# Kernel tuning notes

Hardware: AMD Instinct MI355X
Metric: run time of the kernel (lower is better)

## Reference

```python
import jax, jax.numpy as jnp
import numpy as np
import math

D = 768
H = 8
DK = D // H
FF = 1024
EPS = 1e-5


def _layer_norm(x, g, b):
    m = jnp.mean(x, axis=-1, keepdims=True)
    v = jnp.mean((x - m) ** 2, axis=-1, keepdims=True)
    return (x - m) * jax.lax.rsqrt(v + EPS) * g + b


def _mha(x, attention_mask, Wq, bq, Wv, bv, g, b):
    # x: (B,S,D); attention_mask: (B,S,1) bool (True = masked/padding query row)
    B, S, _ = x.shape
    q = (x @ Wq + bq).reshape(B, S, H, DK).transpose(0, 2, 1, 3)  # (B,H,S,dk)
    # NOTE: original code uses the V projection for BOTH k and v (k = self.V(x))
    kv = (x @ Wv + bv).reshape(B, S, H, DK).transpose(0, 2, 1, 3)
    k = kv
    v = kv
    w = jnp.einsum('bhqd,bhkd->bhqk', q, k) / math.sqrt(DK)  # (B,H,S,S)
    pad = attention_mask[:, None, :, :]                      # (B,1,S,1) -> bcast (B,1,S,S)
    causal = jnp.triu(jnp.ones((S, S), dtype=bool), k=1)     # look-ahead mask
    mask = pad | causal
    w = jnp.where(mask, jnp.float32(-1e9), w)
    # NOTE: original uses nn.Softmax(dim=2) -> softmax over the QUERY axis
    score = jax.nn.softmax(w, axis=2)
    o = jnp.einsum('bhqk,bhkd->bhqd', score, v)              # (B,H,S,dk)
    o = o.transpose(0, 2, 1, 3).reshape(B, S, D)
    return _layer_norm(o + x, g, b)


def _ffn(x, W1, b1, W2, b2, g, b):
    h = jax.nn.relu(x @ W1 + b1)
    return _layer_norm(h @ W2 + b2 + x, g, b)


def setup_inputs() -> dict:
    key = jax.random.key(0)
    ks = jax.random.split(key, 16)
    B, S = 8, 1024
    sc = 0.02
    inp = {
        'x': jax.random.normal(ks[0], (B, S, D), dtype=jnp.float32),
        'attention_mask': jax.random.randint(ks[1], (B, S, 1), 0, 2).astype(bool),
    }
    for i, pre in enumerate(['a1', 'a2']):
        inp[pre + '_Wq'] = jax.random.normal(ks[2 + 4 * i], (D, D), dtype=jnp.float32) * sc
        inp[pre + '_bq'] = jnp.zeros((D,), dtype=jnp.float32)
        inp[pre + '_Wv'] = jax.random.normal(ks[3 + 4 * i], (D, D), dtype=jnp.float32) * sc
        inp[pre + '_bv'] = jnp.zeros((D,), dtype=jnp.float32)
        inp[pre + '_g'] = jnp.ones((D,), dtype=jnp.float32)
        inp[pre + '_b'] = jnp.zeros((D,), dtype=jnp.float32)
    inp['f_W1'] = jax.random.normal(ks[10], (D, FF), dtype=jnp.float32) * sc
    inp['f_b1'] = jnp.zeros((FF,), dtype=jnp.float32)
    inp['f_W2'] = jax.random.normal(ks[11], (FF, D), dtype=jnp.float32) * sc
    inp['f_b2'] = jnp.zeros((D,), dtype=jnp.float32)
    inp['f_g'] = jnp.ones((D,), dtype=jnp.float32)
    inp['f_b'] = jnp.zeros((D,), dtype=jnp.float32)
    return inp


def reference(x, attention_mask,
              a1_Wq, a1_bq, a1_Wv, a1_bv, a1_g, a1_b,
              a2_Wq, a2_bq, a2_Wv, a2_bv, a2_g, a2_b,
              f_W1, f_b1, f_W2, f_b2, f_g, f_b):
    x = _mha(x, attention_mask, a1_Wq, a1_bq, a1_Wv, a1_bv, a1_g, a1_b)
    x = _mha(x, attention_mask, a2_Wq, a2_bq, a2_Wv, a2_bv, a2_g, a2_b)
    x = _ffn(x, f_W1, f_b1, f_W2, f_b2, f_g, f_b)
    return x
```

## Files before the change

kernel.cpp:

```cpp
#include <hip/hip_runtime.h>
#include <cstddef>

#define BB 8
#define SS 1024
#define DD 768
#define HH 8
#define DKK 96
#define FFF 1024
#define MM (BB*SS)
#define QVW 1536
#define SM_SCALE 0.10206207261596577f
#define NT2 8

typedef unsigned short ushort_t;
typedef short short8 __attribute__((ext_vector_type(8)));
typedef float f32x4 __attribute__((ext_vector_type(4)));
typedef float f32x16 __attribute__((ext_vector_type(16)));
typedef ushort_t us4 __attribute__((ext_vector_type(4)));
typedef unsigned uint2v __attribute__((ext_vector_type(2)));

__device__ __forceinline__ ushort_t f2b(float f) {
    union { float f; unsigned u; } x; x.f = f;
    unsigned r = x.u + 0x7fffu + ((x.u >> 16) & 1u);
    return (ushort_t)(r >> 16);
}
__device__ __forceinline__ float b2f(ushort_t u) {
    union { unsigned u; float f; } x; x.u = ((unsigned)u) << 16;
    return x.f;
}
__device__ __forceinline__ void gload16(const ushort_t* g, void* lds_base) {
    __builtin_amdgcn_global_load_lds(
        (const __attribute__((address_space(1))) unsigned int*)g,
        (__attribute__((address_space(3))) unsigned int*)lds_base, 16, 0, 0);
}
__device__ __forceinline__ void plswap(unsigned& a, unsigned& b) {
#if __has_builtin(__builtin_amdgcn_permlane32_swap)
    uint2v r = __builtin_amdgcn_permlane32_swap(a, b, false, false);
    a = r[0]; b = r[1];
#else
    asm("v_permlane32_swap_b32 %0, %1" : "+v"(a), "+v"(b));
#endif
}

__device__ __forceinline__ void castWT_body(
    const float* __restrict__ W, ushort_t* __restrict__ Wt,
    int K, int N, int bx, int by)
{
    __shared__ float T[32][33];
    const int tx = threadIdx.x & 31, ty = threadIdx.x >> 5;
    const int n0 = bx * 32, k0 = by * 32;
    #pragma unroll
    for (int r = 0; r < 4; ++r)
        T[ty + 8*r][tx] = W[(size_t)(k0 + ty + 8*r) * N + n0 + tx];
    __syncthreads();
    #pragma unroll
    for (int r = 0; r < 4; ++r)
        Wt[(size_t)(n0 + ty + 8*r) * K + k0 + tx] = f2b(T[tx][ty + 8*r]);
}

__global__ __launch_bounds__(256) void prep_all(
    const float* __restrict__ Wqa, const float* __restrict__ Wva,
    const float* __restrict__ Wqb, const float* __restrict__ Wvb,
    ushort_t* __restrict__ Tqa, ushort_t* __restrict__ Tva,
    ushort_t* __restrict__ Tqb, ushort_t* __restrict__ Tvb,
    const float* __restrict__ W1, ushort_t* __restrict__ T1,
    const float* __restrict__ W2, ushort_t* __restrict__ T2,
    const float* __restrict__ x, ushort_t* __restrict__ xb)
{
    const int id = blockIdx.x;
    if (id < 2304) {
        const int z = id / 576, r = id % 576;
        const float* W = (z == 0) ? Wqa : (z == 1) ? Wva : (z == 2) ? Wqb : Wvb;
        ushort_t* Wt   = (z == 0) ? Tqa : (z == 1) ? Tva : (z == 2) ? Tqb : Tvb;
        castWT_body(W, Wt, DD, DD, r % 24, r / 24);
    } else if (id < 3072) {
        const int r = id - 2304;
        castWT_body(W1, T1, DD, FFF, r % 32, r / 32);
    } else if (id < 3840) {
        const int r = id - 3072;
        castWT_body(W2, T2, FFF, DD, r % 24, r / 24);
    } else {
        const int i = (id - 3840) * 256 + threadIdx.x;
        const float4 v = ((const float4*)x)[i];
        us4 o; o.x = f2b(v.x); o.y = f2b(v.y); o.z = f2b(v.z); o.w = f2b(v.w);
        ((us4*)xb)[i] = o;
    }
}

template<int RELU>
__global__ __launch_bounds__(256) void gemm_bt(
    const ushort_t* __restrict__ A, const ushort_t* __restrict__ Bt,
    const float* __restrict__ bias, const float* __restrict__ bias2, int bN,
    ushort_t* __restrict__ C, int K, int N)
{
    __shared__ ushort_t S[4*128*64];
    const int tid  = threadIdx.x;
    const int lane = tid & 63, wave = tid >> 6;
    const int wm = wave >> 1, wn = wave & 1;
    const int n = lane & 15, quad = lane >> 4;
    const int sx = n & 7;
    const int nbx = N >> 7;
    const int cpx = gridDim.x >> 3;
    const int sw  = (blockIdx.x & 7) * cpx + (blockIdx.x >> 3);
    const int bm = (sw / nbx) * 128, bn = (sw % nbx) * 128;

    f32x4 acc[4][4];
    #pragma unroll
    for (int i = 0; i < 4; ++i)
        #pragma unroll
        for (int j = 0; j < 4; ++j) acc[i][j] = (f32x4){0.f, 0.f, 0.f, 0.f};

    auto stage = [&](int k0, int buf) {
        char* abase = (char*)S + buf * 16384;
        char* bbase = (char*)S + 32768 + buf * 16384;
        #pragma unroll
        for (int it = 0; it < 4; ++it) {
            const int u   = (it*4 + wave)*64 + lane;
            const int row = u >> 3;
            const int c   = (u & 7) ^ (row & 7);
            gload16(A  + (size_t)(bm + row) * K + k0 + c*8, abase + (it*4 + wave)*1024);
            gload16(Bt + (size_t)(bn + row) * K + k0 + c*8, bbase + (it*4 + wave)*1024);
        }
    };

    stage(0, 0);
    __syncthreads();
    int cur = 0;
    for (int k0 = 0; k0 < K; k0 += 64) {
        if (k0 + 64 < K) stage(k0 + 64, cur ^ 1);
        const ushort_t* As = S + cur * 8192;
        const ushort_t* Bs = S + 16384 + cur * 8192;
        #pragma unroll
        for (int ks = 0; ks < 2; ++ks) {
            short8 af[4], bf[4];
            #pragma unroll
            for (int i = 0; i < 4; ++i)
                af[i] = *(short8*)&As[((wm*64 + i*16 + n)*8 + ((ks*4 + quad) ^ sx))*8];
            #pragma unroll
            for (int j = 0; j < 4; ++j)
                bf[j] = *(short8*)&Bs[((wn*64 + j*16 + n)*8 + ((ks*4 + quad) ^ sx))*8];
            __builtin_amdgcn_s_setprio(1);
            #pragma unroll
            for (int i = 0; i < 4; ++i)
                #pragma unroll
                for (int j = 0; j < 4; ++j)
                    acc[i][j] = __builtin_amdgcn_mfma_f32_16x16x32_bf16(af[i], bf[j], acc[i][j], 0, 0, 0);
            __builtin_amdgcn_s_setprio(0);
        }
        __syncthreads();
        cur ^= 1;
    }
    #pragma unroll
    for (int j = 0; j < 4; ++j) {
        const int col = wn*64 + j*16 + n;
        const int gcol = bn + col;
        const float bsv = (gcol < bN) ? bias[gcol] : bias2[gcol - bN];
        #pragma unroll
        for (int i = 0; i < 4; ++i) {
            const int lrow = wm*64 + i*16 + quad*4;
            #pragma unroll
            for (int r = 0; r < 4; ++r) {
                float v = acc[i][j][r] + bsv;
                if (RELU) v = fmaxf(v, 0.f);
                S[(lrow + r)*136 + col] = f2b(v);
            }
        }
    }
    __syncthreads();
    #pragma unroll
    for (int it = 0; it < 8; ++it) {
        const int u = it*256 + tid;
        const int grow = u >> 4, gc = u & 15;
        *(short8*)(C + (size_t)(bm + grow)*N + bn + gc*8) = *(short8*)&S[grow*136 + gc*8];
    }
}

__global__ __launch_bounds__(512) void attn_sums(
    const ushort_t* __restrict__ QV, const int* __restrict__ amask,
    float* __restrict__ lpart)
{
    __shared__ ushort_t Qs[128*128];
    __shared__ ushort_t Ks[2][64*128];
    __shared__ float colsum[2][8][64];
    const int tid = threadIdx.x, lane = tid & 63, wave = tid >> 6;
    const int n = lane & 15, quad = lane >> 4, sx = n & 7;
    const int hwid = blockIdx.x;
    const int v = (hwid & 7) * 32 + (hwid >> 3);
    const int px = v & 3, h = (v >> 2) & 7, b = v >> 5;
    const ushort_t* Qh = QV + (size_t)b*SS*QVW + h*DKK;
    const ushort_t* Kh = QV + (size_t)b*SS*QVW + DD + h*DKK;
    float* lpq = lpart + (size_t)(b*HH + h)*NT2*SS;

    #pragma unroll
    for (int half = 0; half < 2; ++half) {
        const int qt2 = half ? (7 - px) : px;
        const int q0 = qt2 * 128;
        const int ktmax = 2*qt2 + 1;
        #pragma unroll
        for (int it = 0; it < 4; ++it) {
            const int u = (it*8 + wave)*64 + lane;
            const int row = u >> 4, c = (u & 15) ^ (row & 7);
            if (c < 12)
                gload16(Qh + (size_t)(q0 + row)*QVW + c*8, (char*)Qs + (it*8 + wave)*1024);
        }
        const int4 mv = *(const int4*)&amask[b*SS + q0 + wave*16 + quad*4];
        const int mr[4] = {mv.x, mv.y, mv.z, mv.w};
        #pragma unroll
        for (int it = 0; it < 2; ++it) {
            const int u = (it*8 + wave)*64 + lane;
            const int row = u >> 4, c = (u & 15) ^ (row & 7);
            if (c < 12)
                gload16(Kh + (size_t)row*QVW + c*8, (char*)Ks[0] + (it*8 + wave)*1024);
        }
        __syncthreads();
        short8 aq[3];
        #pragma unroll
        for (int ks = 0; ks < 3; ++ks)
            aq[ks] = *(short8*)&Qs[((wave*16 + n)*16 + ((ks*4 + quad) ^ sx))*8];

        int cur = 0;
        for (int kt = 0; kt <= ktmax; ++kt) {
            const int k0 = kt * 64;
            if (kt < ktmax) {
                #pragma unroll
                for (int it = 0; it < 2; ++it) {
                    const int u = (it*8 + wave)*64 + lane;
                    const int row = u >> 4, c = (u & 15) ^ (row & 7);
                    if (c < 12)
                        gload16(Kh + (size_t)(k0 + 64 + row)*QVW + c*8,
                                (char*)Ks[cur^1] + (it*8 + wave)*1024);
                }
            }
            if (kt > 0 && tid < 64) {
                const float s = colsum[cur^1][0][tid] + colsum[cur^1][1][tid]
                              + colsum[cur^1][2][tid] + colsum[cur^1][3][tid]
                              + colsum[cur^1][4][tid] + colsum[cur^1][5][tid]
                              + colsum[cur^1][6][tid] + colsum[cur^1][7][tid];
                lpq[(size_t)qt2*SS + (k0 - 64) + tid] = s;
            }
            #pragma unroll
            for (int ns = 0; ns < 4; ++ns) {
                f32x4 sa = (f32x4){0.f, 0.f, 0.f, 0.f};
                __builtin_amdgcn_s_setprio(1);
                #pragma unroll
                for (int ks = 0; ks < 3; ++ks) {
                    const short8 bk = *(short8*)&Ks[cur][((ns*16 + n)*16 + ((ks*4 + quad) ^ sx))*8];
                    sa = __builtin_amdgcn_mfma_f32_16x16x32_bf16(aq[ks], bk, sa, 0, 0, 0);
                }
                __builtin_amdgcn_s_setprio(0);
                const int kl = ns*16 + n;
                const int keyg = k0 + kl;
                float s = 0.f;
                #pragma unroll
                for (int r = 0; r < 4; ++r) {
                    const int qg = q0 + wave*16 + quad*4 + r;
                    const bool dead = (mr[r] != 0) || (keyg > qg);
                    s += dead ? 0.f : __expf(sa[r] * SM_SCALE);
                }
                s += __shfl_xor(s, 16);
                s += __shfl_xor(s, 32);
                if (quad == 0) colsum[cur][wave][kl] = s;
            }
            __syncthreads();
            cur ^= 1;
        }
        if (tid < 64) {
            const int pb = ktmax & 1;
            const float s = colsum[pb][0][tid] + colsum[pb][1][tid]
                          + colsum[pb][2][tid] + colsum[pb][3][tid]
                          + colsum[pb][4][tid] + colsum[pb][5][tid]
                          + colsum[pb][6][tid] + colsum[pb][7][tid];
            lpq[(size_t)qt2*SS + ktmax*64 + tid] = s;
        }
    }
}

__global__ __launch_bounds__(256) void transpose_scale(
    const ushort_t* __restrict__ QV, const float* __restrict__ lpart,
    ushort_t* __restrict__ Vt)
{
    __shared__ ushort_t T[64][104];
    __shared__ float rlv[64];
    const int tid = threadIdx.x;
    const int k0 = blockIdx.x * 64, h = blockIdx.y, b = blockIdx.z;
    const ushort_t* src = QV + (size_t)b*SS*QVW + DD + h*DKK;
    for (int s = tid; s < 768; s += 256) {
        const int r = s / 12, c = s % 12;
        *(short8*)&T[r][c*8] = *(const short8*)(src + (size_t)(k0 + r)*QVW + c*8);
    }
    if (tid < 64) {
        const float* lp = lpart + (size_t)(b*HH + h)*NT2*SS;
        float l = 0.f;
        for (int qt2 = k0 >> 7; qt2 < NT2; ++qt2) l += lp[(size_t)qt2*SS + k0 + tid];
        rlv[tid] = (l > 0.f) ? (1.f / l) : 0.f;
    }
    __syncthreads();
    ushort_t* dst = Vt + ((size_t)b*HH + h)*DKK*SS;
    for (int s = tid; s < 768; s += 256) {
        const int dk = s >> 3, c = s & 7;
        short8 v;
        #pragma unroll
        for (int i = 0; i < 8; ++i)
            v[i] = (short)f2b(b2f(T[c*8 + i][dk]) * rlv[c*8 + i]);
        *(short8*)(dst + (size_t)dk*SS + k0 + c*8) = v;
    }
}

__global__ __launch_bounds__(512, 1) void attn_pv_re(
    const ushort_t* __restrict__ QV, const int* __restrict__ amask,
    const ushort_t* __restrict__ Vt, ushort_t* __restrict__ O)
{
    __shared__ ushort_t Ks[2][2][64*128];
    __shared__ ushort_t Vs[2][2][96*64];
    const int tid = threadIdx.x, lane = tid & 63, wave = tid >> 6;
    const int grp = wave >> 2, w4 = wave & 3;
    const int ln31 = lane & 31, hi = lane >> 5;
    const int hwid = blockIdx.x;
    const int v = (hwid & 7) * 32 + (hwid >> 3);
    const int px = v & 3, h = (v >> 2) & 7, b = v >> 5;
    const ushort_t* Qh = QV + (size_t)b*SS*QVW + h*DKK;
    const ushort_t* Kh = QV + (size_t)b*SS*QVW + DD + h*DKK;
    const ushort_t* Vth = Vt + ((size_t)b*HH + h)*DKK*SS;

    const int qt2 = grp ? (7 - px) : px;
    const int q0 = qt2 * 128;
    const int ktmax = 2*qt2 + 1;
    const int ktend = 2*(7 - px) + 1;
    const int qrow = q0 + w4*32 + ln31;
    short8 bq[6];
    #pragma unroll
    for (int t = 0; t < 6; ++t)
        bq[t] = *(const short8*)(Qh + (size_t)qrow*QVW + t*16 + hi*8);
    const bool padq = amask[b*SS + qrow] != 0;

    #pragma unroll
    for (int it = 0; it < 4; ++it) {
        const int u = (it*4 + w4)*64 + lane;
        const int row = u >> 4, c = (u & 15) ^ (row & 7);
        if (c < 12)
            gload16(Kh + (size_t)row*QVW + c*8, (char*)Ks[grp][0] + (it*4 + w4)*1024);
    }
    #pragma unroll
    for (int it = 0; it < 3; ++it) {
        const int u = (it*4 + w4)*64 + lane;
        const int row = u >> 3, c = (u & 7) ^ (row & 7);
        gload16(Vth + (size_t)row*SS + c*8, (char*)Vs[grp][0] + (it*4 + w4)*1024);
    }
    __syncthreads();

    f32x16 acc[3];
    #pragma unroll
    for (int db = 0; db < 3; ++db)
        #pragma unroll
        for (int i = 0; i < 16; ++i) acc[db][i] = 0.f;

    int cur = 0;
    for (int kt = 0; kt <= ktend; ++kt) {
        const int k0 = kt * 64;
        if (kt < ktmax) {
            #pragma unroll
            for (int it = 0; it < 4; ++it) {
                const int u = (it*4 + w4)*64 + lane;
                const int row = u >> 4, c = (u & 15) ^ (row & 7);
                if (c < 12)
                    gload16(Kh + (size_t)(k0 + 64 + row)*QVW + c*8,
                            (char*)Ks[grp][cur^1] + (it*4 + w4)*1024);
            }
            #pragma unroll
            for (int it = 0; it < 3; ++it) {
                const int u = (it*4 + w4)*64 + lane;
                const int row = u >> 3, c = (u & 7) ^ (row & 7);
                gload16(Vth + (size_t)row*SS + k0 + 64 + c*8,
                        (char*)Vs[grp][cur^1] + (it*4 + w4)*1024);
            }
        }
        if (kt <= ktmax) {
            #pragma unroll
            for (int kb = 0; kb < 2; ++kb) {
                f32x16 sk;
                #pragma unroll
                for (int i = 0; i < 16; ++i) sk[i] = 0.f;
                const int krow = kb*32 + ln31;
                __builtin_amdgcn_s_setprio(1);
                #pragma unroll
                for (int t = 0; t < 6; ++t) {
                    const short8 ak = *(short8*)&Ks[grp][cur][krow*128 + (((t*2 + hi) ^ (krow & 7))*8)];
                    sk = __builtin_amdgcn_mfma_f32_32x32x16_bf16(ak, bq[t], sk, 0, 0, 0);
                }
                __builtin_amdgcn_s_setprio(0);
                const int kbase = k0 + kb*32 + 4*hi;
                float p[16];
                #pragma unroll
                for (int r = 0; r < 16; ++r) {
                    const int kg = kbase + (r & 3) + 8*(r >> 2);
                    const bool dead = padq || (kg > qrow);
                    p[r] = dead ? 0.f : __expf(sk[r] * SM_SCALE);
                }
                unsigned w[8];
                #pragma unroll
                for (int i = 0; i < 8; ++i)
                    asm("v_cvt_pk_bf16_f32 %0, %1, %2" : "=v"(w[i]) : "v"(p[2*i]), "v"(p[2*i+1]));
                plswap(w[0], w[2]);
                plswap(w[1], w[3]);
                plswap(w[4], w[6]);
                plswap(w[5], w[7]);
                __builtin_amdgcn_s_setprio(1);
                #pragma unroll
                for (int s = 0; s < 2; ++s) {
                    short8 ae;
                    unsigned* aeu = (unsigned*)&ae;
                    aeu[0] = w[s*4 + 0]; aeu[1] = w[s*4 + 1];
                    aeu[2] = w[s*4 + 2]; aeu[3] = w[s*4 + 3];
                    #pragma unroll
                    for (int db = 0; db < 3; ++db) {
                        const int drow = db*32 + ln31;
                        const short8 bv = *(short8*)&Vs[grp][cur][drow*64 + (((kb*4 + s*2 + hi) ^ (drow & 7))*8)];
                        acc[db] = __builtin_amdgcn_mfma_f32_32x32x16_bf16(ae, bv, acc[db], 0, 0, 0);
                    }
                }
                __builtin_amdgcn_s_setprio(0);
            }
        }
        __syncthreads();
        cur ^= 1;
    }
    #pragma unroll
    for (int db = 0; db < 3; ++db) {
        #pragma unroll
        for (int r = 0; r < 16; ++r) {
            const int q = q0 + w4*32 + (r & 3) + 8*(r >> 2) + 4*hi;
            O[((size_t)b*SS + q)*DD + h*DKK + db*32 + ln31] = f2b(acc[db][r]);
        }
    }
}

__device__ __forceinline__ float block_sum256(float s, float* tmp4)
{
    #pragma unroll
    for (int off = 32; off > 0; off >>= 1) s += __shfl_down(s, off);
    __syncthreads();
    if ((threadIdx.x & 63) == 0) tmp4[threadIdx.x >> 6] = s;
    __syncthreads();
    return tmp4[0] + tmp4[1] + tmp4[2] + tmp4[3];
}

template<int XBF, int RBF, int OUTF32>
__global__ __launch_bounds__(256) void resid_ln(
    const void* __restrict__ X, const void* __restrict__ R,
    const float* __restrict__ g, const float* __restrict__ beta,
    ushort_t* __restrict__ OutB, float* __restrict__ OutF)
{
    __shared__ float tmp4[4];
    const int row = blockIdx.x;
    const int tid = threadIdx.x;
    float v[3], s = 0.f;
    #pragma unroll
    for (int i = 0; i < 3; ++i) {
        const size_t idx = (size_t)row * DD + tid + 256*i;
        const float xv = XBF ? b2f(((const ushort_t*)X)[idx]) : ((const float*)X)[idx];
        const float rv = RBF ? b2f(((const ushort_t*)R)[idx]) : ((const float*)R)[idx];
        v[i] = xv + rv;
        s += v[i];
    }
    const float mu = block_sum256(s, tmp4) * (1.f / DD);
    float qv = 0.f;
    #pragma unroll
    for (int i = 0; i < 3; ++i) { const float d = v[i] - mu; qv += d * d; }
    const float inv = rsqrtf(block_sum256(qv, tmp4) * (1.f / DD) + 1e-5f);
    #pragma unroll
    for (int i = 0; i < 3; ++i) {
        const int c = tid + 256*i;
        const float o = (v[i] - mu) * inv * g[c] + beta[c];
        if (OUTF32) OutF[(size_t)row * DD + c] = o;
        else        OutB[(size_t)row * DD + c] = f2b(o);
    }
}

extern "C" void kernel_launch(void* const* d_in, const int* in_sizes, int n_in,
                              void* d_out, int out_size, void* d_ws, size_t ws_size,
                              hipStream_t stream)
{
    (void)in_sizes; (void)n_in; (void)out_size; (void)ws_size;
    const float* x0    = (const float*)d_in[0];
    const int*   amask = (const int*)d_in[1];
    const float* a1_Wq = (const float*)d_in[2];
    const float* a1_bq = (const float*)d_in[3];
    const float* a1_Wv = (const float*)d_in[4];
    const float* a1_bv = (const float*)d_in[5];
    const float* a1_g  = (const float*)d_in[6];
    const float* a1_b  = (const float*)d_in[7];
    const float* a2_Wq = (const float*)d_in[8];
    const float* a2_bq = (const float*)d_in[9];
    const float* a2_Wv = (const float*)d_in[10];
    const float* a2_bv = (const float*)d_in[11];
    const float* a2_g  = (const float*)d_in[12];
    const float* a2_b  = (const float*)d_in[13];
    const float* f_W1  = (const float*)d_in[14];
    const float* f_b1  = (const float*)d_in[15];
    const float* f_W2  = (const float*)d_in[16];
    const float* f_b2  = (const float*)d_in[17];
    const float* f_g   = (const float*)d_in[18];
    const float* f_b   = (const float*)d_in[19];

    char* ws = (char*)d_ws;
    size_t off = 0;
    auto alloc = [&](size_t bytes) { void* p = ws + off; off += (bytes + 255) & ~(size_t)255; return p; };
    ushort_t* WqvT1 = (ushort_t*)alloc((size_t)QVW*DD*2);
    ushort_t* WqvT2 = (ushort_t*)alloc((size_t)QVW*DD*2);
    ushort_t* W1T   = (ushort_t*)alloc((size_t)DD*FFF*2);
    ushort_t* W2T   = (ushort_t*)alloc((size_t)DD*FFF*2);
    ushort_t* xb0   = (ushort_t*)alloc((size_t)MM*DD*2);
    ushort_t* xb1   = (ushort_t*)alloc((size_t)MM*DD*2);
    ushort_t* xb2   = (ushort_t*)alloc((size_t)MM*DD*2);
    ushort_t* Ob    = (ushort_t*)alloc((size_t)MM*DD*2);
    ushort_t* QVb   = (ushort_t*)alloc((size_t)MM*QVW*2);
    ushort_t* hb    = QVb;
    ushort_t* Vtb   = (ushort_t*)alloc((size_t)MM*DD*2);
    float* lpart = (float*)alloc((size_t)BB*HH*NT2*SS*4);
    float* out = (float*)d_out;

    const dim3 blk(256);
    const dim3 blk512(512);
    const dim3 gat(256);
    const dim3 gtr(SS/64, HH, BB);

    prep_all<<<dim3(9984), blk, 0, stream>>>(
        a1_Wq, a1_Wv, a2_Wq, a2_Wv,
        WqvT1, WqvT1 + (size_t)DD*DD, WqvT2, WqvT2 + (size_t)DD*DD,
        f_W1, W1T, f_W2, W2T, x0, xb0);

    gemm_bt<0><<<dim3((QVW/128)*(MM/128)), blk, 0, stream>>>(xb0, WqvT1, a1_bq, a1_bv, DD, QVb, DD, QVW);
    attn_sums<<<gat, blk512, 0, stream>>>(QVb, amask, lpart);
    transpose_scale<<<gtr, blk, 0, stream>>>(QVb, lpart, Vtb);
    attn_pv_re<<<gat, blk512, 0, stream>>>(QVb, amask, Vtb, Ob);
    resid_ln<1,0,0><<<dim3(MM), blk, 0, stream>>>(Ob, x0, a1_g, a1_b, xb1, nullptr);

    gemm_bt<0><<<dim3((QVW/128)*(MM/128)), blk, 0, stream>>>(xb1, WqvT2, a2_bq, a2_bv, DD, QVb, DD, QVW);
    attn_sums<<<gat, blk512, 0, stream>>>(QVb, amask, lpart);
    transpose_scale<<<gtr, blk, 0, stream>>>(QVb, lpart, Vtb);
    attn_pv_re<<<gat, blk512, 0, stream>>>(QVb, amask, Vtb, Ob);
    resid_ln<1,1,0><<<dim3(MM), blk, 0, stream>>>(Ob, xb1, a2_g, a2_b, xb2, nullptr);

    gemm_bt<1><<<dim3((FFF/128)*(MM/128)), blk, 0, stream>>>(xb2, W1T, f_b1, f_b1, FFF, hb, DD, FFF);
    gemm_bt<0><<<dim3((DD/128)*(MM/128)), blk, 0, stream>>>(hb, W2T, f_b2, f_b2, DD, Ob, FFF, DD);
    resid_ln<1,1,1><<<dim3(MM), blk, 0, stream>>>(Ob, xb2, f_g, f_b, nullptr, out);
}
```

Baseline: 372.4 us.

## Restructure attn_sums into two concurrent wave groups with 32x32 MFMA tiles

The column-sum kernel previously processed its two query tiles one after another, using eight waves with 16x16 MFMAs and Q staged through shared memory. Now two groups of four waves each take one query tile concurrently, with their own double-buffered K tiles. Q fragments load straight into registers and scores come from 32x32x16 MFMAs. Both attention kernels also split the dot-product accumulation across two independent accumulators to break the MFMA dependency chain. The trade-off is an unbalanced group workload (the short tile idles at barriers), more registers with launch_bounds(512,1), and extra adds before the exp.

After: 377.9 us. No clear change (+1.5%).

```diff
diff --git a/kernel.cpp b/kernel.cpp
--- a/kernel.cpp
+++ b/kernel.cpp
@@ -175,15 +175,15 @@
     }
 }
 
-__global__ __launch_bounds__(512) void attn_sums(
+__global__ __launch_bounds__(512, 1) void attn_sums(
     const ushort_t* __restrict__ QV, const int* __restrict__ amask,
     float* __restrict__ lpart)
 {
-    __shared__ ushort_t Qs[128*128];
-    __shared__ ushort_t Ks[2][64*128];
-    __shared__ float colsum[2][8][64];
+    __shared__ ushort_t Ks[2][2][64*128];
+    __shared__ float colsum[2][2][4][64];
     const int tid = threadIdx.x, lane = tid & 63, wave = tid >> 6;
-    const int n = lane & 15, quad = lane >> 4, sx = n & 7;
+    const int grp = wave >> 2, w4 = wave & 3;
+    const int ln31 = lane & 31, hi = lane >> 5;
     const int hwid = blockIdx.x;
     const int v = (hwid & 7) * 32 + (hwid >> 3);
     const int px = v & 3, h = (v >> 2) & 7, b = v >> 5;
@@ -191,87 +191,81 @@
     const ushort_t* Kh = QV + (size_t)b*SS*QVW + DD + h*DKK;
     float* lpq = lpart + (size_t)(b*HH + h)*NT2*SS;
 
-    #pragma unroll
-    for (int half = 0; half < 2; ++half) {
-        const int qt2 = half ? (7 - px) : px;
-        const int q0 = qt2 * 128;
-        const int ktmax = 2*qt2 + 1;
-        #pragma unroll
-        for (int it = 0; it < 4; ++it) {
-            const int u = (it*8 + wave)*64 + lane;
-            const int row = u >> 4, c = (u & 15) ^ (row & 7);
-            if (c < 12)
-                gload16(Qh + (size_t)(q0 + row)*QVW + c*8, (char*)Qs + (it*8 + wave)*1024);
-        }
-        const int4 mv = *(const int4*)&amask[b*SS + q0 + wave*16 + quad*4];
-        const int mr[4] = {mv.x, mv.y, mv.z, mv.w};
-        #pragma unroll
-        for (int it = 0; it < 2; ++it) {
-            const int u = (it*8 + wave)*64 + lane;
-            const int row = u >> 4, c = (u & 15) ^ (row & 7);
-            if (c < 12)
-                gload16(Kh + (size_t)row*QVW + c*8, (char*)Ks[0] + (it*8 + wave)*1024);
-        }
-        __syncthreads();
-        short8 aq[3];
-        #pragma unroll
-        for (int ks = 0; ks < 3; ++ks)
-            aq[ks] = *(short8*)&Qs[((wave*16 + n)*16 + ((ks*4 + quad) ^ sx))*8];
-
-        int cur = 0;
-        for (int kt = 0; kt <= ktmax; ++kt) {
-            const int k0 = kt * 64;
-            if (kt < ktmax) {
-                #pragma unroll
-                for (int it = 0; it < 2; ++it) {
-                    const int u = (it*8 + wave)*64 + lane;
-                    const int row = u >> 4, c = (u & 15) ^ (row & 7);
-                    if (c < 12)
-                        gload16(Kh + (size_t)(k0 + 64 + row)*QVW + c*8,
-                                (char*)Ks[cur^1] + (it*8 + wave)*1024);
-                }
+    const int qt2 = grp ? (7 - px) : px;
+    const int q0 = qt2 * 128;
+    const int ktmax = 2*qt2 + 1;
+    const int ktend = 2*(7 - px) + 1;
+    short8 aq[6];
+    #pragma unroll
+    for (int t = 0; t < 6; ++t)
+        aq[t] = *(const short8*)(Qh + (size_t)(q0 + w4*32 + ln31)*QVW + t*16 + hi*8);
+    int4 mr[4];
+    #pragma unroll
+    for (int m = 0; m < 4; ++m)
+        mr[m] = *(const int4*)&amask[b*SS + q0 + w4*32 + 8*m + 4*hi];
+
+    #pragma unroll
+    for (int it = 0; it < 4; ++it) {
+        const int u = (it*4 + w4)*64 + lane;
+        const int row = u >> 4, c = (u & 15) ^ (row & 7);
+        if (c < 12)
+            gload16(Kh + (size_t)row*QVW + c*8, (char*)Ks[grp][0] + (it*4 + w4)*1024);
+    }
+    __syncthreads();
+
+    int cur = 0;
+    for (int kt = 0; kt <= ktend; ++kt) {
+        const int k0 = kt * 64;
+        if (kt < ktmax) {
+            #pragma unroll
+            for (int it = 0; it < 4; ++it) {
+                const int u = (it*4 + w4)*64 + lane;
+                const int row = u >> 4, c = (u & 15) ^ (row & 7);
+                if (c < 12)
+                    gload16(Kh + (size_t)(k0 + 64 + row)*QVW + c*8,
+                            (char*)Ks[grp][cur^1] + (it*4 + w4)*1024);
             }
-            if (kt > 0 && tid < 64) {
-                const float s = colsum[cur^1][0][tid] + colsum[cur^1][1][tid]
-                              + colsum[cur^1][2][tid] + colsum[cur^1][3][tid]
-                              + colsum[cur^1][4][tid] + colsum[cur^1][5][tid]
-                              + colsum[cur^1][6][tid] + colsum[cur^1][7][tid];
-                lpq[(size_t)qt2*SS + (k0 - 64) + tid] = s;
-            }
-            #pragma unroll
-            for (int ns = 0; ns < 4; ++ns) {
-                f32x4 sa = (f32x4){0.f, 0.f, 0.f, 0.f};
+        }
+        if (kt > 0 && kt <= ktmax + 1 && w4 == 0) {
+            const float s = colsum[grp][cur^1][0][lane] + colsum[grp][cur^1][1][lane]
+                          + colsum[grp][cur^1][2][lane] + colsum[grp][cur^1][3][lane];
+            lpq[(size_t)qt2*SS + (k0 - 64) + lane] = s;
+        }
+        if (kt <= ktmax) {
+            #pragma unroll
+            for (int kb = 0; kb < 2; ++kb) {
+                f32x16 s0, s1;
+                #pragma unroll
+                for (int i = 0; i < 16; ++i) { s0[i] = 0.f; s1[i] = 0.f; }
+                const int krow = kb*32 + ln31;
                 __builtin_amdgcn_s_setprio(1);
                 #pragma unroll
-                for (int ks = 0; ks < 3; ++ks) {
-                    const short8 bk = *(short8*)&Ks[cur][((ns*16 + n)*16 + ((ks*4 + quad) ^ sx))*8];
-                    sa = __builtin_amdgcn_mfma_f32_16x16x32_bf16(aq[ks], bk, sa, 0, 0, 0);
+                for (int t = 0; t < 6; ++t) {
+                    const short8 bk = *(short8*)&Ks[grp][cur][krow*128 + (((t*2 + hi) ^ (krow & 7))*8)];
+                    if (t & 1) s1 = __builtin_amdgcn_mfma_f32_32x32x16_bf16(aq[t], bk, s1, 0, 0, 0);
+                    else       s0 = __builtin_amdgcn_mfma_f32_32x32x16_bf16(aq[t], bk, s0, 0, 0, 0);
                 }
                 __builtin_amdgcn_s_setprio(0);
-                const int kl = ns*16 + n;
-                const int keyg = k0 + kl;
+                const int keyg = k0 + kb*32 + ln31;
                 float s = 0.f;
                 #pragma unroll
-                for (int r = 0; r < 4; ++r) {
-                    const int qg = q0 + wave*16 + quad*4 + r;
-                    const bool dead = (mr[r] != 0) || (keyg > qg);
-                    s += dead ? 0.f : __expf(sa[r] * SM_SCALE);
+                for (int r = 0; r < 16; ++r) {
+                    const int qg = q0 + w4*32 + (r & 3) + 8*(r >> 2) + 4*hi;
+                    const bool dead = ((&mr[r >> 2].x)[r & 3] != 0) || (keyg > qg);
+                    s += dead ? 0.f : __expf((s0[r] + s1[r]) * SM_SCALE);
                 }
-                s += __shfl_xor(s, 16);
                 s += __shfl_xor(s, 32);
-                if (quad == 0) colsum[cur][wave][kl] = s;
+                if (hi == 0) colsum[grp][cur][w4][kb*32 + ln31] = s;
             }
-            __syncthreads();
-            cur ^= 1;
-        }
-        if (tid < 64) {
-            const int pb = ktmax & 1;
-            const float s = colsum[pb][0][tid] + colsum[pb][1][tid]
-                          + colsum[pb][2][tid] + colsum[pb][3][tid]
-                          + colsum[pb][4][tid] + colsum[pb][5][tid]
-                          + colsum[pb][6][tid] + colsum[pb][7][tid];
-            lpq[(size_t)qt2*SS + ktmax*64 + tid] = s;
-        }
+        }
+        __syncthreads();
+        cur ^= 1;
+    }
+    if (grp == 1 && w4 == 0) {
+        const int pb = ktend & 1;
+        const float s = colsum[1][pb][0][lane] + colsum[1][pb][1][lane]
+                      + colsum[1][pb][2][lane] + colsum[1][pb][3][lane];
+        lpq[(size_t)qt2*SS + ktend*64 + lane] = s;
     }
 }
 
@@ -377,15 +371,16 @@
         if (kt <= ktmax) {
             #pragma unroll
             for (int kb = 0; kb < 2; ++kb) {
-                f32x16 sk;
-                #pragma unroll
-                for (int i = 0; i < 16; ++i) sk[i] = 0.f;
+                f32x16 s0, s1;
+                #pragma unroll
+                for (int i = 0; i < 16; ++i) { s0[i] = 0.f; s1[i] = 0.f; }
                 const int krow = kb*32 + ln31;
                 __builtin_amdgcn_s_setprio(1);
                 #pragma unroll
                 for (int t = 0; t < 6; ++t) {
                     const short8 ak = *(short8*)&Ks[grp][cur][krow*128 + (((t*2 + hi) ^ (krow & 7))*8)];
-                    sk = __builtin_amdgcn_mfma_f32_32x32x16_bf16(ak, bq[t], sk, 0, 0, 0);
+                    if (t & 1) s1 = __builtin_amdgcn_mfma_f32_32x32x16_bf16(ak, bq[t], s1, 0, 0, 0);
+                    else       s0 = __builtin_amdgcn_mfma_f32_32x32x16_bf16(ak, bq[t], s0, 0, 0, 0);
                 }
                 __builtin_amdgcn_s_setprio(0);
                 const int kbase = k0 + kb*32 + 4*hi;
@@ -394,7 +389,7 @@
                 for (int r = 0; r < 16; ++r) {
                     const int kg = kbase + (r & 3) + 8*(r >> 2);
                     const bool dead = padq || (kg > qrow);
-                    p[r] = dead ? 0.f : __expf(sk[r] * SM_SCALE);
+                    p[r] = dead ? 0.f : __expf((s0[r] + s1[r]) * SM_SCALE);
                 }
                 unsigned w[8];
                 #pragma unroll
```
